# Kernel optimization log

Measured on AMD Instinct MI355X. Metric: run time of the kernel, lower is better.

## Reference

```python
import jax, jax.numpy as jnp
import numpy as np

B, C, D = 8192, 10000, 128
CLAMP_MIN, CLAMP_MAX = 1e-12, 1e12


def setup_inputs() -> dict:
    key = jax.random.key(0)
    k1, k2, k3 = jax.random.split(key, 3)
    x = jax.random.normal(k1, (B, D), dtype=jnp.float32)
    labels = jax.random.randint(k2, (B,), 0, C, dtype=jnp.int64)
    centers = jax.random.normal(k3, (C, D), dtype=jnp.float32)
    lr = jnp.array([0.1], dtype=jnp.float32)
    return {"x": x, "labels": labels, "centers": centers, "lr": lr}


def reference(x, labels, centers, lr):
    b, d = x.shape
    c = centers.shape[0]
    # --- vectorized center update (replaces double python loop) ---
    # A_j = count_j * centers[j] - sum_{i: labels_i==j} x_i ; delta_j = A_j / (1 + count_j)
    counts = jax.ops.segment_sum(jnp.ones((b,), dtype=x.dtype), labels, num_segments=c)  # [C]
    sum_x = jax.ops.segment_sum(x, labels, num_segments=c)                               # [C, D]
    delta = (counts[:, None] * centers - sum_x) / (1.0 + counts[:, None])
    centers = centers - lr * delta
    # --- squared euclidean distance matrix [B, C] ---
    distmat = (
        jnp.sum(x * x, axis=1, keepdims=True)
        + jnp.sum(centers * centers, axis=1)[None, :]
        - 2.0 * (x @ centers.T)
    )
    git = 1.0 / (1.0 + distmat)
    # gather own-class entries (replaces per-sample mask loop)
    lab = labels[:, None]
    center_vals = jnp.take_along_axis(distmat, lab, axis=1)[:, 0]          # [B]
    git_vals = jnp.sum(git, axis=1) - jnp.take_along_axis(git, lab, axis=1)[:, 0]
    center_loss = jnp.mean(jnp.clip(center_vals, CLAMP_MIN, CLAMP_MAX))
    git_loss = jnp.mean(jnp.clip(git_vals, CLAMP_MIN, CLAMP_MAX))
    return (center_loss, git_loss)
```

## Files before the change

### kernel.cpp

```cpp
#include <hip/hip_runtime.h>
#include <hip/hip_bf16.h>

#define B_ 8192
#define C_ 10000
#define D_ 128
#define CPAD 10112
#define NPADC 112
#define NT_TOT 158
#define NSTRIP 16
#define STRIPW 10
#define UPD_BLOCKS 2528
#define CVAL_BLOCKS 2048

typedef float f32x4 __attribute__((ext_vector_type(4)));
typedef short s16x8 __attribute__((ext_vector_type(8)));

typedef const __attribute__((address_space(1))) uint32_t gu32;
typedef __attribute__((address_space(3))) uint32_t lu32;


__global__ void zero_ws(float4* __restrict__ ws, float* __restrict__ out) {
    int idx = blockIdx.x * 256 + threadIdx.x;
    if (idx < 324608) ws[idx] = float4{0.f, 0.f, 0.f, 0.f};
    if (idx == 0) { out[0] = 0.f; out[1] = 0.f; }
}

__global__ void scatter_prep(const float* __restrict__ x, const int* __restrict__ labels,
                             float* __restrict__ counts, float* __restrict__ sumx,
                             float* __restrict__ xnorm, __hip_bfloat16* __restrict__ xb) {
    int tid = threadIdx.x;
    int w = tid >> 6, lane = tid & 63;
    int i = blockIdx.x * 4 + w;
    int l = labels[i];
    float2 v = *(const float2*)&x[i * D_ + lane * 2];
    atomicAdd(&sumx[l * D_ + lane * 2], v.x);
    atomicAdd(&sumx[l * D_ + lane * 2 + 1], v.y);
    if (lane == 0) atomicAdd(&counts[l], 1.0f);
    __hip_bfloat162 p;
    p.x = __float2bfloat16(v.x);
    p.y = __float2bfloat16(v.y);
    *(__hip_bfloat162*)&xb[i * D_ + lane * 2] = p;
    float s = v.x * v.x + v.y * v.y;
    #pragma unroll
    for (int m = 1; m < 64; m <<= 1) s += __shfl_xor(s, m);
    if (lane == 0) xnorm[i] = s;
}

__global__ void upd_cvals(const float* __restrict__ centers, const float* __restrict__ counts,
                          const float* __restrict__ sumx, float* __restrict__ cnorm,
                          __hip_bfloat16* __restrict__ cb, const float* __restrict__ lr,
                          const float* __restrict__ x, const int* __restrict__ labels,
                          float* __restrict__ cent_val) {
    int tid = threadIdx.x;
    int w = tid >> 6, lane = tid & 63;
    int bid = blockIdx.x;
    float lrv = lr[0];

    if (bid < UPD_BLOCKS) {
        int c = bid * 4 + w;
        if (c >= C_) {
            *(uint*)&cb[c * D_ + lane * 2] = 0u;
            if (lane == 0) cnorm[c] = 0.0f;
            return;
        }
        float cnt = counts[c];
        float2 cv = *(const float2*)&centers[c * D_ + lane * 2];
        float2 sx = *(const float2*)&sumx[c * D_ + lane * 2];
        float inv = 1.0f / (1.0f + cnt);
        float nx = cv.x - lrv * (cnt * cv.x - sx.x) * inv;
        float ny = cv.y - lrv * (cnt * cv.y - sx.y) * inv;
        __hip_bfloat162 p;
        p.x = __float2bfloat16(nx);
        p.y = __float2bfloat16(ny);
        *(__hip_bfloat162*)&cb[c * D_ + lane * 2] = p;
        float s = nx * nx + ny * ny;
        #pragma unroll
        for (int m = 1; m < 64; m <<= 1) s += __shfl_xor(s, m);
        if (lane == 0) cnorm[c] = s;
    } else {
        int i = (bid - UPD_BLOCKS) * 4 + w;
        int l = labels[i];
        float cnt = counts[l];
        float inv = 1.0f / (1.0f + cnt);
        float2 a  = *(const float2*)&x[i * D_ + lane * 2];
        float2 cv = *(const float2*)&centers[l * D_ + lane * 2];
        float2 sx = *(const float2*)&sumx[l * D_ + lane * 2];
        float nx = cv.x - lrv * (cnt * cv.x - sx.x) * inv;
        float ny = cv.y - lrv * (cnt * cv.y - sx.y) * inv;
        float dx = a.x - nx, dy = a.y - ny;
        float s = dx * dx + dy * dy;
        #pragma unroll
        for (int m = 1; m < 64; m <<= 1) s += __shfl_xor(s, m);
        if (lane == 0) cent_val[i] = s;
    }
}

__global__ void __launch_bounds__(256, 2)
gemm_git(const __hip_bfloat16* __restrict__ xb, const __hip_bfloat16* __restrict__ cb,
         const float* __restrict__ xnorm, const float* __restrict__ cnorm,
         float* __restrict__ git_row) {
    __shared__ char ldsB[3][16384];
    __shared__ float cnLDS[STRIPW * 64];

    int tid = threadIdx.x;
    int w = tid >> 6, lane = tid & 63;
    int lr_ = lane & 15, lg = lane >> 4;
    int bm = blockIdx.x;
    int strip = blockIdx.y;
    int row0 = bm * 256 + w * 64;
    int bn0 = strip * STRIPW;
    int nt = (strip == NSTRIP - 1) ? (NT_TOT - bn0) : STRIPW;

    const s16x8* gx = (const s16x8*)xb;

    s16x8 af[4][4];
    #pragma unroll
    for (int kk = 0; kk < 4; kk++)
        #pragma unroll
        for (int f = 0; f < 4; f++) {
            uint4 u = __builtin_bit_cast(uint4, gx[(row0 + f * 16 + lr_) * 16 + kk * 4 + lg]);
            asm volatile("" : "+v"(u.x), "+v"(u.y), "+v"(u.z), "+v"(u.w));
            af[kk][f] = __builtin_bit_cast(s16x8, u);
        }

    float xn1[4][4];
    #pragma unroll
    for (int fm = 0; fm < 4; fm++)
        #pragma unroll
        for (int r = 0; r < 4; r++) {
            float v = 1.0f + xnorm[row0 + fm * 16 + lg * 4 + r];
            asm volatile("" : "+v"(v));
            xn1[fm][r] = v;
        }

    float gitsum[4][4] = {};

    const char* gB = (const char*)cb;
    size_t goff[4];
    #pragma unroll
    for (int p = 0; p < 4; p++) {
        int s = tid + p * 256;
        int sr = s >> 4, sc = (s & 15) ^ (sr & 7);
        goff[p] = (size_t)(sr * 16 + sc) * 16;
    }

    auto stage = [&](int t, int buf) {
        const char* base = gB + (size_t)(bn0 + t) * 64 * 256;
        #pragma unroll
        for (int p = 0; p < 4; p++)
            __builtin_amdgcn_global_load_lds((gu32*)(base + goff[p]),
                                             (lu32*)&ldsB[buf][(tid + p * 256) * 16], 16, 0, 0);
    };

    for (int i = tid; i < nt * 64; i += 256) cnLDS[i] = cnorm[bn0 * 64 + i];
    stage(0, 0);
    if (nt > 1) stage(1, 1);
    __syncthreads();

    for (int t = 0; t < nt; ++t) {
        int bc = t % 3;
        if (t + 2 < nt) stage(t + 2, (t + 2) % 3);

        if (t + 2 < nt)      asm volatile("s_waitcnt vmcnt(8)" ::: "memory");
        else if (t + 1 < nt) asm volatile("s_waitcnt vmcnt(4)" ::: "memory");
        else                 asm volatile("s_waitcnt vmcnt(0)" ::: "memory");
        __builtin_amdgcn_sched_barrier(0);
        __builtin_amdgcn_s_barrier();
        __builtin_amdgcn_sched_barrier(0);

        float cn[4];
        #pragma unroll
        for (int fn = 0; fn < 4; fn++) cn[fn] = cnLDS[t * 64 + fn * 16 + lr_];

        f32x4 acc[4][4] = {};
        __builtin_amdgcn_s_setprio(1);
        #pragma unroll
        for (int kk = 0; kk < 4; kk++) {
            s16x8 bfk[4];
            int kc = kk * 4 + lg;
            #pragma unroll
            for (int fn = 0; fn < 4; fn++) {
                int row = fn * 16 + lr_;
                int ch = kc ^ (lr_ & 7);
                bfk[fn] = *(const s16x8*)&ldsB[bc][(row * 16 + ch) * 16];
            }
            #pragma unroll
            for (int fm = 0; fm < 4; fm++)
                #pragma unroll
                for (int fn = 0; fn < 4; fn++)
                    acc[fm][fn] = __builtin_amdgcn_mfma_f32_16x16x32_bf16(af[kk][fm], bfk[fn], acc[fm][fn], 0, 0, 0);
        }
        __builtin_amdgcn_s_setprio(0);

        #pragma unroll
        for (int fm = 0; fm < 4; fm++)
            #pragma unroll
            for (int r = 0; r < 4; r++) {
                float base = xn1[fm][r];
                #pragma unroll
                for (int fp = 0; fp < 4; fp += 2) {
                    float u = base + cn[fp]     - 2.0f * acc[fm][fp][r];
                    float v = base + cn[fp + 1] - 2.0f * acc[fm][fp + 1][r];
                    gitsum[fm][r] += (u + v) * __builtin_amdgcn_rcpf(u * v);
                }
            }

        __builtin_amdgcn_sched_barrier(0);
        __builtin_amdgcn_s_barrier();
        __builtin_amdgcn_sched_barrier(0);
    }

    #pragma unroll
    for (int fm = 0; fm < 4; fm++)
        #pragma unroll
        for (int r = 0; r < 4; r++) {
            float s = gitsum[fm][r];
            s += __shfl_xor(s, 1); s += __shfl_xor(s, 2);
            s += __shfl_xor(s, 4); s += __shfl_xor(s, 8);
            if (lr_ == 0) atomicAdd(&git_row[row0 + fm * 16 + lg * 4 + r], s);
        }
}

__global__ void final_reduce(const float* __restrict__ cent_val, const float* __restrict__ git_row,
                             const float* __restrict__ xnorm, float* __restrict__ out) {
    int tid = threadIdx.x;
    int i = blockIdx.x * 256 + tid;
    float c = cent_val[i];
    float cl = fminf(fmaxf(c, 1e-12f), 1e12f);
    float g = git_row[i] - 1.0f / (1.0f + c) - (float)NPADC / (1.0f + xnorm[i]);
    float gl = fminf(fmaxf(g, 1e-12f), 1e12f);
    #pragma unroll
    for (int m = 1; m < 64; m <<= 1) { cl += __shfl_xor(cl, m); gl += __shfl_xor(gl, m); }
    __shared__ float scl[4], sgl[4];
    if ((tid & 63) == 0) { scl[tid >> 6] = cl; sgl[tid >> 6] = gl; }
    __syncthreads();
    if (tid == 0) {
        float a = scl[0] + scl[1] + scl[2] + scl[3];
        float b = sgl[0] + sgl[1] + sgl[2] + sgl[3];
        atomicAdd(&out[0], a / (float)B_);
        atomicAdd(&out[1], b / (float)B_);
    }
}

extern "C" void kernel_launch(void* const* d_in, const int* in_sizes, int n_in,
                              void* d_out, int out_size, void* d_ws, size_t ws_size,
                              hipStream_t stream) {
    const float* x       = (const float*)d_in[0];
    const int*   labels  = (const int*)d_in[1];
    const float* centers = (const float*)d_in[2];
    const float* lr      = (const float*)d_in[3];

    float* ws       = (float*)d_ws;
    float* counts   = ws;
    float* sumx     = ws + 10240;
    float* git_row  = ws + 1290240;
    float* xnorm    = ws + 1298432;
    float* cent_val = ws + 1306624;
    float* cnorm    = ws + 1314816;
    __hip_bfloat16* xb = (__hip_bfloat16*)((char*)d_ws + 5300224);
    __hip_bfloat16* cb = (__hip_bfloat16*)((char*)d_ws + 7397376);
    float* out = (float*)d_out;

    zero_ws<<<1268, 256, 0, stream>>>((float4*)d_ws, out);
    scatter_prep<<<B_ / 4, 256, 0, stream>>>(x, labels, counts, sumx, xnorm, xb);
    upd_cvals<<<UPD_BLOCKS + CVAL_BLOCKS, 256, 0, stream>>>(centers, counts, sumx, cnorm, cb, lr,
                                                            x, labels, cent_val);
    gemm_git<<<dim3(32, NSTRIP), 256, 0, stream>>>(xb, cb, xnorm, cnorm, git_row);
    final_reduce<<<32, 256, 0, stream>>>(cent_val, git_row, xnorm, out);
}
```

Before: 58.04 us.

## Switch distance GEMM from bf16 to fp8 e4m3 scaled MFMA

```diff
diff --git a/kernel.cpp b/kernel.cpp
--- a/kernel.cpp
+++ b/kernel.cpp
@@ -1,5 +1,6 @@
 #include <hip/hip_runtime.h>
 #include <hip/hip_bf16.h>
+#include <hip/hip_fp8.h>
 
 #define B_ 8192
 #define C_ 10000
@@ -13,7 +14,7 @@
 #define CVAL_BLOCKS 2048
 
 typedef float f32x4 __attribute__((ext_vector_type(4)));
-typedef short s16x8 __attribute__((ext_vector_type(8)));
+typedef int   i32x8 __attribute__((ext_vector_type(8)));
 
 typedef const __attribute__((address_space(1))) uint32_t gu32;
 typedef __attribute__((address_space(3))) uint32_t lu32;
@@ -27,7 +28,7 @@
 
 __global__ void scatter_prep(const float* __restrict__ x, const int* __restrict__ labels,
                              float* __restrict__ counts, float* __restrict__ sumx,
-                             float* __restrict__ xnorm, __hip_bfloat16* __restrict__ xb) {
+                             float* __restrict__ xnorm, unsigned char* __restrict__ xb8) {
     int tid = threadIdx.x;
     int w = tid >> 6, lane = tid & 63;
     int i = blockIdx.x * 4 + w;
@@ -36,10 +37,9 @@
     atomicAdd(&sumx[l * D_ + lane * 2], v.x);
     atomicAdd(&sumx[l * D_ + lane * 2 + 1], v.y);
     if (lane == 0) atomicAdd(&counts[l], 1.0f);
-    __hip_bfloat162 p;
-    p.x = __float2bfloat16(v.x);
-    p.y = __float2bfloat16(v.y);
-    *(__hip_bfloat162*)&xb[i * D_ + lane * 2] = p;
+    __hip_fp8_e4m3 a(v.x), b(v.y);
+    unsigned short pk = (unsigned short)a.__x | ((unsigned short)b.__x << 8);
+    *(unsigned short*)&xb8[i * D_ + lane * 2] = pk;
     float s = v.x * v.x + v.y * v.y;
     #pragma unroll
     for (int m = 1; m < 64; m <<= 1) s += __shfl_xor(s, m);
@@ -48,7 +48,7 @@
 
 __global__ void upd_cvals(const float* __restrict__ centers, const float* __restrict__ counts,
                           const float* __restrict__ sumx, float* __restrict__ cnorm,
-                          __hip_bfloat16* __restrict__ cb, const float* __restrict__ lr,
+                          unsigned char* __restrict__ cb8, const float* __restrict__ lr,
                           const float* __restrict__ x, const int* __restrict__ labels,
                           float* __restrict__ cent_val) {
     int tid = threadIdx.x;
@@ -59,7 +59,7 @@
     if (bid < UPD_BLOCKS) {
         int c = bid * 4 + w;
         if (c >= C_) {
-            *(uint*)&cb[c * D_ + lane * 2] = 0u;
+            *(unsigned short*)&cb8[c * D_ + lane * 2] = 0;
             if (lane == 0) cnorm[c] = 0.0f;
             return;
         }
@@ -69,10 +69,9 @@
         float inv = 1.0f / (1.0f + cnt);
         float nx = cv.x - lrv * (cnt * cv.x - sx.x) * inv;
         float ny = cv.y - lrv * (cnt * cv.y - sx.y) * inv;
-        __hip_bfloat162 p;
-        p.x = __float2bfloat16(nx);
-        p.y = __float2bfloat16(ny);
-        *(__hip_bfloat162*)&cb[c * D_ + lane * 2] = p;
+        __hip_fp8_e4m3 a(nx), b(ny);
+        unsigned short pk = (unsigned short)a.__x | ((unsigned short)b.__x << 8);
+        *(unsigned short*)&cb8[c * D_ + lane * 2] = pk;
         float s = nx * nx + ny * ny;
         #pragma unroll
         for (int m = 1; m < 64; m <<= 1) s += __shfl_xor(s, m);
@@ -96,10 +95,10 @@
 }
 
 __global__ void __launch_bounds__(256, 2)
-gemm_git(const __hip_bfloat16* __restrict__ xb, const __hip_bfloat16* __restrict__ cb,
+gemm_git(const unsigned char* __restrict__ xb8, const unsigned char* __restrict__ cb8,
          const float* __restrict__ xnorm, const float* __restrict__ cnorm,
          float* __restrict__ git_row) {
-    __shared__ char ldsB[3][16384];
+    __shared__ char ldsB[3][8192];
     __shared__ float cnLDS[STRIPW * 64];
 
     int tid = threadIdx.x;
@@ -111,17 +110,16 @@
     int bn0 = strip * STRIPW;
     int nt = (strip == NSTRIP - 1) ? (NT_TOT - bn0) : STRIPW;
 
-    const s16x8* gx = (const s16x8*)xb;
-
-    s16x8 af[4][4];
-    #pragma unroll
-    for (int kk = 0; kk < 4; kk++)
-        #pragma unroll
-        for (int f = 0; f < 4; f++) {
-            uint4 u = __builtin_bit_cast(uint4, gx[(row0 + f * 16 + lr_) * 16 + kk * 4 + lg]);
-            asm volatile("" : "+v"(u.x), "+v"(u.y), "+v"(u.z), "+v"(u.w));
-            af[kk][f] = __builtin_bit_cast(s16x8, u);
-        }
+    i32x8 af[4];
+    #pragma unroll
+    for (int f = 0; f < 4; f++) {
+        const uint4* pa = (const uint4*)(xb8 + (size_t)(row0 + f * 16 + lr_) * 128 + lg * 32);
+        uint4 u0 = pa[0], u1 = pa[1];
+        asm volatile("" : "+v"(u0.x), "+v"(u0.y), "+v"(u0.z), "+v"(u0.w),
+                          "+v"(u1.x), "+v"(u1.y), "+v"(u1.z), "+v"(u1.w));
+        af[f] = i32x8{(int)u0.x, (int)u0.y, (int)u0.z, (int)u0.w,
+                      (int)u1.x, (int)u1.y, (int)u1.z, (int)u1.w};
+    }
 
     float xn1[4][4];
     #pragma unroll
@@ -135,21 +133,18 @@
 
     float gitsum[4][4] = {};
 
-    const char* gB = (const char*)cb;
-    size_t goff[4];
-    #pragma unroll
-    for (int p = 0; p < 4; p++) {
-        int s = tid + p * 256;
-        int sr = s >> 4, sc = (s & 15) ^ (sr & 7);
-        goff[p] = (size_t)(sr * 16 + sc) * 16;
-    }
+    const char* gB = (const char*)cb8;
+    int sr0 = tid >> 3,          sc0 = (tid & 7) ^ (sr0 & 7);
+    int sr1 = (tid + 256) >> 3,  sc1 = ((tid + 256) & 7) ^ (sr1 & 7);
+    size_t goff0 = (size_t)sr0 * 128 + sc0 * 16;
+    size_t goff1 = (size_t)sr1 * 128 + sc1 * 16;
 
     auto stage = [&](int t, int buf) {
-        const char* base = gB + (size_t)(bn0 + t) * 64 * 256;
-        #pragma unroll
-        for (int p = 0; p < 4; p++)
-            __builtin_amdgcn_global_load_lds((gu32*)(base + goff[p]),
-                                             (lu32*)&ldsB[buf][(tid + p * 256) * 16], 16, 0, 0);
+        const char* base = gB + (size_t)(bn0 + t) * 64 * 128;
+        __builtin_amdgcn_global_load_lds((gu32*)(base + goff0),
+                                         (lu32*)&ldsB[buf][tid * 16], 16, 0, 0);
+        __builtin_amdgcn_global_load_lds((gu32*)(base + goff1),
+                                         (lu32*)&ldsB[buf][4096 + tid * 16], 16, 0, 0);
     };
 
     for (int i = tid; i < nt * 64; i += 256) cnLDS[i] = cnorm[bn0 * 64 + i];
@@ -161,8 +156,8 @@
         int bc = t % 3;
         if (t + 2 < nt) stage(t + 2, (t + 2) % 3);
 
-        if (t + 2 < nt)      asm volatile("s_waitcnt vmcnt(8)" ::: "memory");
-        else if (t + 1 < nt) asm volatile("s_waitcnt vmcnt(4)" ::: "memory");
+        if (t + 2 < nt)      asm volatile("s_waitcnt vmcnt(4)" ::: "memory");
+        else if (t + 1 < nt) asm volatile("s_waitcnt vmcnt(2)" ::: "memory");
         else                 asm volatile("s_waitcnt vmcnt(0)" ::: "memory");
         __builtin_amdgcn_sched_barrier(0);
         __builtin_amdgcn_s_barrier();
@@ -171,25 +166,29 @@
         float cn[4];
         #pragma unroll
         for (int fn = 0; fn < 4; fn++) cn[fn] = cnLDS[t * 64 + fn * 16 + lr_];
+
+        i32x8 bfk[4];
+        int r7 = lr_ & 7;
+        #pragma unroll
+        for (int fn = 0; fn < 4; fn++) {
+            const char* rowp = &ldsB[bc][(fn * 16 + lr_) * 128];
+            uint4 q0 = *(const uint4*)(rowp + (((lg * 2)     ^ r7) * 16));
+            uint4 q1 = *(const uint4*)(rowp + (((lg * 2 + 1) ^ r7) * 16));
+            bfk[fn] = i32x8{(int)q0.x, (int)q0.y, (int)q0.z, (int)q0.w,
+                            (int)q1.x, (int)q1.y, (int)q1.z, (int)q1.w};
+        }
 
         f32x4 acc[4][4] = {};
         __builtin_amdgcn_s_setprio(1);
         #pragma unroll
-        for (int kk = 0; kk < 4; kk++) {
-            s16x8 bfk[4];
-            int kc = kk * 4 + lg;
+        for (int fm = 0; fm < 4; fm++)
             #pragma unroll
-            for (int fn = 0; fn < 4; fn++) {
-                int row = fn * 16 + lr_;
-                int ch = kc ^ (lr_ & 7);
-                bfk[fn] = *(const s16x8*)&ldsB[bc][(row * 16 + ch) * 16];
-            }
-            #pragma unroll
-            for (int fm = 0; fm < 4; fm++)
-                #pragma unroll
-                for (int fn = 0; fn < 4; fn++)
-                    acc[fm][fn] = __builtin_amdgcn_mfma_f32_16x16x32_bf16(af[kk][fm], bfk[fn], acc[fm][fn], 0, 0, 0);
-        }
+            for (int fn = 0; fn < 4; fn++)
+                acc[fm][fn] = __builtin_amdgcn_mfma_scale_f32_16x16x128_f8f6f4(
+                    af[fm], bfk[fn], acc[fm][fn],
+                    0, 0,
+                    0, 0x7F,
+                    0, 0x7F);
         __builtin_amdgcn_s_setprio(0);
 
         #pragma unroll
@@ -257,14 +256,14 @@
     float* xnorm    = ws + 1298432;
     float* cent_val = ws + 1306624;
     float* cnorm    = ws + 1314816;
-    __hip_bfloat16* xb = (__hip_bfloat16*)((char*)d_ws + 5300224);
-    __hip_bfloat16* cb = (__hip_bfloat16*)((char*)d_ws + 7397376);
+    unsigned char* xb8 = (unsigned char*)d_ws + 5300224;
+    unsigned char* cb8 = (unsigned char*)d_ws + 7397376;
     float* out = (float*)d_out;
 
     zero_ws<<<1268, 256, 0, stream>>>((float4*)d_ws, out);
-    scatter_prep<<<B_ / 4, 256, 0, stream>>>(x, labels, counts, sumx, xnorm, xb);
-    upd_cvals<<<UPD_BLOCKS + CVAL_BLOCKS, 256, 0, stream>>>(centers, counts, sumx, cnorm, cb, lr,
+    scatter_prep<<<B_ / 4, 256, 0, stream>>>(x, labels, counts, sumx, xnorm, xb8);
+    upd_cvals<<<UPD_BLOCKS + CVAL_BLOCKS, 256, 0, stream>>>(centers, counts, sumx, cnorm, cb8, lr,
                                                             x, labels, cent_val);
-    gemm_git<<<dim3(32, NSTRIP), 256, 0, stream>>>(xb, cb, xnorm, cnorm, git_row);
+    gemm_git<<<dim3(32, NSTRIP), 256, 0, stream>>>(xb8, cb8, xnorm, cnorm, git_row);
     final_reduce<<<32, 256, 0, stream>>>(cent_val, git_row, xnorm, out);
 }
```

Measured after the change: 50.29 us. 1.15x faster.
